# Performance work log

Measured on AMD Instinct MI355X. Metric: run time of the kernel, lower is better.

Reference implementation:

```python
import jax, jax.numpy as jnp
import numpy as np

B, S, H = 1, 4096, 2048
NH, HD = 16, 128
ROPE_N = 32
WINDOW = 1024
EPS = 1e-5


def _build_rope(seq_len, n_elem, base=10000.0):
    theta = 1.0 / (base ** (np.arange(0, n_elem, 2, dtype=np.float32) / n_elem))  # [n_elem/2]
    idx = np.arange(seq_len, dtype=np.float32)
    freqs = np.outer(idx, theta)                     # [S, n_elem/2]
    freqs = np.concatenate([freqs, freqs], axis=-1)  # [S, n_elem]
    return jnp.asarray(np.cos(freqs)), jnp.asarray(np.sin(freqs))


def setup_inputs() -> dict:
    key = jax.random.key(0)
    k1, k2, k3 = jax.random.split(key, 3)
    x = jax.random.normal(k1, (B, S, H), dtype=jnp.float32)
    cos, sin = _build_rope(S, ROPE_N)
    norm_weight = jnp.ones((H,), dtype=jnp.float32)
    qkv_w = jax.random.normal(k2, (3 * H, H), dtype=jnp.float32) * (1.0 / np.sqrt(H))
    o_w = jax.random.normal(k3, (H, H), dtype=jnp.float32) * (1.0 / np.sqrt(H))
    return {"x": x, "cos": cos, "sin": sin, "norm_weight": norm_weight,
            "qkv_w": qkv_w, "o_w": o_w}


def _apply_rope(t, cos, sin):
    # t: [B, NH, S, ROPE_N]; cos/sin: [S, ROPE_N]
    half = t.shape[-1] // 2
    x1, x2 = t[..., :half], t[..., half:]
    rotated = jnp.concatenate([-x2, x1], axis=-1)
    return t * cos + rotated * sin


def reference(x, cos, sin, norm_weight, qkv_w, o_w):
    b, s, h = x.shape
    # RMSNorm (computed in fp32)
    xf = x.astype(jnp.float32)
    ms = jnp.mean(xf * xf, axis=-1, keepdims=True)
    xn = (norm_weight * (xf * jax.lax.rsqrt(ms + EPS))).astype(x.dtype)
    # fused QKV projection
    qkv = jnp.einsum('bsh,oh->bso', xn, qkv_w)  # [B, S, 3H]
    q, k, v = jnp.split(qkv, 3, axis=-1)
    def to_heads(t):
        return t.reshape(b, s, NH, HD).transpose(0, 2, 1, 3)  # [B, NH, S, HD]
    q, k, v = to_heads(q), to_heads(k), to_heads(v)
    # partial RoPE on first ROPE_N dims
    q = jnp.concatenate([_apply_rope(q[..., :ROPE_N], cos, sin), q[..., ROPE_N:]], axis=-1)
    k = jnp.concatenate([_apply_rope(k[..., :ROPE_N], cos, sin), k[..., ROPE_N:]], axis=-1)
    # sliding-window causal attention: query i attends keys j with i-WINDOW <= j <= i
    scale = 1.0 / np.sqrt(HD)
    scores = jnp.einsum('bnqd,bnkd->bnqk', q, k) * scale  # [B, NH, S, S]
    i = jnp.arange(s)[:, None]
    j = jnp.arange(s)[None, :]
    mask = (j <= i) & (j >= i - WINDOW)
    scores = jnp.where(mask, scores, jnp.finfo(scores.dtype).min)
    attn = jax.nn.softmax(scores, axis=-1)
    out = jnp.einsum('bnqk,bnkd->bnqd', attn, v)  # [B, NH, S, HD]
    out = out.transpose(0, 2, 1, 3).reshape(b, s, h)
    return jnp.einsum('bsh,oh->bso', out, o_w)
```

## Files before the change

### kernel.cpp

```cpp
#include <hip/hip_runtime.h>
#include <stdint.h>

#define S_LEN 4096
#define HDIM  2048
#define NHEAD 16
#define HD    128
#define WIN   1024

typedef float  f32x4  __attribute__((ext_vector_type(4)));
typedef float  f32x4v __attribute__((ext_vector_type(4)));
typedef __bf16 bf16x8 __attribute__((ext_vector_type(8)));
typedef short  short8 __attribute__((ext_vector_type(8)));
typedef short  short4v __attribute__((ext_vector_type(4)));

static __device__ __forceinline__ short f2bf(float f) {
  union { float f; uint32_t u; } v; v.f = f;
  uint32_t r = (v.u + 0x7FFFu + ((v.u >> 16) & 1u)) >> 16;
  return (short)(uint16_t)r;
}

static __device__ __forceinline__ void gload_lds16(const void* g, void* l) {
  __builtin_amdgcn_global_load_lds((__attribute__((address_space(1))) void*)g,
                                   (__attribute__((address_space(3))) void*)l,
                                   16, 0, 0);
}

__global__ __launch_bounds__(256) void rmsnorm_k(const float* __restrict__ x,
                                                 const float* __restrict__ w,
                                                 short* __restrict__ xn) {
  const int row = blockIdx.x;
  const int t = threadIdx.x;
  const float* xr = x + (size_t)row * HDIM;
  f32x4v a = *(const f32x4v*)&xr[t * 8];
  f32x4v b = *(const f32x4v*)&xr[t * 8 + 4];
  float ss = a.x*a.x + a.y*a.y + a.z*a.z + a.w*a.w
           + b.x*b.x + b.y*b.y + b.z*b.z + b.w*b.w;
#pragma unroll
  for (int d = 1; d < 64; d <<= 1) ss += __shfl_xor(ss, d, 64);
  __shared__ float sred[4];
  if ((t & 63) == 0) sred[t >> 6] = ss;
  __syncthreads();
  float tot = sred[0] + sred[1] + sred[2] + sred[3];
  float rs = rsqrtf(tot * (1.0f / HDIM) + 1e-5f);
  float vv[8] = {a.x, a.y, a.z, a.w, b.x, b.y, b.z, b.w};
  const float* wp = w + t * 8;
  short8 o;
#pragma unroll
  for (int j = 0; j < 8; ++j) o[j] = f2bf(vv[j] * rs * wp[j]);
  *(short8*)&xn[(size_t)row * HDIM + t * 8] = o;
}

__global__ __launch_bounds__(256) void cvt_k(const float* __restrict__ in,
                                             short* __restrict__ out, int n4) {
  int i = blockIdx.x * 256 + threadIdx.x;
  if (i >= n4) return;
  f32x4v v = *(const f32x4v*)&in[(size_t)i * 4];
  short4v o = { f2bf(v.x), f2bf(v.y), f2bf(v.z), f2bf(v.w) };
  *(short4v*)&out[(size_t)i * 4] = o;
}

template <int EPI>
__global__ __launch_bounds__(256) void gemm_bt(
    const short* __restrict__ A, const short* __restrict__ Bt,
    int M, int N, int K, float* __restrict__ Cf,
    const float* __restrict__ cosb, const float* __restrict__ sinb,
    short* __restrict__ Qo, short* __restrict__ Ko, short* __restrict__ Vt) {
  __shared__ __align__(16) short Al[128 * 64];
  __shared__ __align__(16) short Bl[128 * 64];
  const int t = threadIdx.x;
  const int w = t >> 6, l = t & 63;
  const int lr = l & 15, lg = l >> 4;
  const int wr = w >> 1, wc = w & 1;
  const int brow = blockIdx.y * 128, bcol = blockIdx.x * 128;

  f32x4 acc[4][4] = {};

  const int srow = t >> 3;
  const int scol = (t & 7) * 8;
  const size_t abase = (size_t)(brow + srow) * K + scol;
  const size_t bbase = (size_t)(bcol + srow) * K + scol;

  for (int kt = 0; kt < K; kt += 64) {
#pragma unroll
    for (int i = 0; i < 4; ++i)
      gload_lds16(A + abase + (size_t)(i * 32) * K + kt, &Al[i * 2048 + w * 512]);
#pragma unroll
    for (int i = 0; i < 4; ++i)
      gload_lds16(Bt + bbase + (size_t)(i * 32) * K + kt, &Bl[i * 2048 + w * 512]);
    __syncthreads();
#pragma unroll
    for (int kk = 0; kk < 2; ++kk) {
      bf16x8 af[4], bfm[4];
#pragma unroll
      for (int m = 0; m < 4; ++m)
        af[m] = *(const bf16x8*)&Al[(wr * 64 + m * 16 + lr) * 64 + kk * 32 + lg * 8];
#pragma unroll
      for (int n = 0; n < 4; ++n)
        bfm[n] = *(const bf16x8*)&Bl[(wc * 64 + n * 16 + lr) * 64 + kk * 32 + lg * 8];
#pragma unroll
      for (int m = 0; m < 4; ++m)
#pragma unroll
        for (int n = 0; n < 4; ++n)
          acc[m][n] = __builtin_amdgcn_mfma_f32_16x16x32_bf16(af[m], bfm[n], acc[m][n], 0, 0, 0);
    }
    __syncthreads();
  }

  const int row0 = brow + wr * 64, col0 = bcol + wc * 64;
  if (EPI == 0) {
#pragma unroll
    for (int m = 0; m < 4; ++m)
#pragma unroll
      for (int n = 0; n < 4; ++n)
#pragma unroll
        for (int r = 0; r < 4; ++r)
          Cf[(size_t)(row0 + m * 16 + lg * 4 + r) * N + col0 + n * 16 + lr] = acc[m][n][r];
  } else {
    const int sec = col0 >> 11;
    const int headc = (col0 & 2047) >> 7;
    const bool rope = (sec < 2) && ((col0 & 127) == 0);
#pragma unroll
    for (int m = 0; m < 4; ++m) {
#pragma unroll
      for (int r = 0; r < 4; ++r) {
        const int s = row0 + m * 16 + lg * 4 + r;
        float v0 = acc[m][0][r], v1 = acc[m][1][r];
        float v2 = acc[m][2][r], v3 = acc[m][3][r];
        if (rope) {
          const int d0 = lr;
          float c0 = cosb[s * 32 + d0],      sn0 = sinb[s * 32 + d0];
          float c1 = cosb[s * 32 + d0 + 16], sn1 = sinb[s * 32 + d0 + 16];
          float t0 = v0 * c0 - v1 * sn0;
          float t1 = v1 * c1 + v0 * sn1;
          v0 = t0; v1 = t1;
        }
        float vv[4] = {v0, v1, v2, v3};
#pragma unroll
        for (int n = 0; n < 4; ++n) {
          const int col = col0 + n * 16 + lr;
          const int d = col & 127;
          if (sec == 0)
            Qo[((size_t)headc * S_LEN + s) * HD + d] = f2bf(vv[n] * 0.08838834764831845f);
          else if (sec == 1)
            Ko[((size_t)headc * S_LEN + s) * HD + d] = f2bf(vv[n]);
          else
            Vt[((size_t)headc * HD + d) * S_LEN + s] = f2bf(vv[n]);
        }
      }
    }
  }
}

__global__ __launch_bounds__(256) void attn_k(const short* __restrict__ Q,
                                              const short* __restrict__ Kk,
                                              const short* __restrict__ Vt,
                                              short* __restrict__ Ao) {
  __shared__ __align__(16) short Kl[64 * HD];
  __shared__ __align__(16) short Vl[HD * 64];
  __shared__ __align__(16) short Pl[4][16 * 72];
  const int head = blockIdx.y;
  int bxx = blockIdx.x;
  bxx = ((bxx & 7) << 3) | (bxx >> 3);
  const int qb = bxx * 64;
  const int w = threadIdx.x >> 6, l = threadIdx.x & 63;
  const int lr = l & 15, lg = l >> 4;
  const int q0w = qb + w * 16;
  const short* Qh = Q  + (size_t)head * S_LEN * HD;
  const short* Kh = Kk + (size_t)head * S_LEN * HD;
  const short* Vh = Vt + (size_t)head * HD * S_LEN;

  bf16x8 qf[4];
#pragma unroll
  for (int kk = 0; kk < 4; ++kk)
    qf[kk] = *(const bf16x8*)&Qh[(size_t)(q0w + lr) * HD + kk * 32 + lg * 8];

  f32x4 oacc[8] = {};
  float mrow[4], lrow[4];
#pragma unroll
  for (int r = 0; r < 4; ++r) { mrow[r] = -1e30f; lrow[r] = 0.0f; }

  const int k_begin = (qb >= WIN) ? (qb - WIN) : 0;
  const int nt = (qb + 64 - k_begin) >> 6;
  const int swz = (lr & 7) << 4;

  for (int tkv = 0; tkv < nt; ++tkv) {
    const int k0 = k_begin + tkv * 64;
#pragma unroll
    for (int i = 0; i < 4; ++i) {
      const int row = i * 16 + w * 4 + (l >> 4);
      gload_lds16(Kh + (size_t)(k0 + row) * HD + (((l & 15) ^ (row & 7)) * 8),
                  &Kl[(i * 16 + w * 4) * HD]);
    }
#pragma unroll
    for (int i = 0; i < 4; ++i) {
      const int row = i * 32 + w * 8 + (l >> 3);
      gload_lds16(Vh + (size_t)row * S_LEN + k0 + (((l & 7) ^ (row & 7)) * 8),
                  &Vl[(i * 32 + w * 8) * 64]);
    }
    __syncthreads();

    f32x4 sacc[4] = {};
#pragma unroll
    for (int nf = 0; nf < 4; ++nf) {
      const char* kb = (const char*)Kl + (nf * 16 + lr) * 256;
      bf16x8 kf[4];
#pragma unroll
      for (int kk = 0; kk < 4; ++kk)
        kf[kk] = *(const bf16x8*)(kb + ((kk * 64 + lg * 16) ^ swz));
#pragma unroll
      for (int kk = 0; kk < 4; ++kk)
        sacc[nf] = __builtin_amdgcn_mfma_f32_16x16x32_bf16(qf[kk], kf[nf == nf ? kk : kk], sacc[nf], 0, 0, 0);
    }

    const bool full = (k0 + 63 <= q0w) && (k0 >= q0w + 15 - WIN);
    float scl[4];
#pragma unroll
    for (int r = 0; r < 4; ++r) {
      const int i = q0w + lg * 4 + r;
      float sv[4];
#pragma unroll
      for (int nf = 0; nf < 4; ++nf) sv[nf] = sacc[nf][r];
      if (!full) {
#pragma unroll
        for (int nf = 0; nf < 4; ++nf) {
          const int j = k0 + nf * 16 + lr;
          if (!((j <= i) && (j + WIN >= i))) sv[nf] = -1e30f;
        }
      }
      float mx = fmaxf(fmaxf(sv[0], sv[1]), fmaxf(sv[2], sv[3]));
#pragma unroll
      for (int d = 1; d < 16; d <<= 1) mx = fmaxf(mx, __shfl_xor(mx, d, 64));
      const float mn = fmaxf(mrow[r], mx);
      const float sc = __expf(mrow[r] - mn);
      mrow[r] = mn;
      float p[4], rs = 0.0f;
#pragma unroll
      for (int nf = 0; nf < 4; ++nf) { p[nf] = __expf(sv[nf] - mn); rs += p[nf]; }
#pragma unroll
      for (int d = 1; d < 16; d <<= 1) rs += __shfl_xor(rs, d, 64);
      lrow[r] = lrow[r] * sc + rs;
      scl[r] = sc;
#pragma unroll
      for (int nf = 0; nf < 4; ++nf)
        Pl[w][(lg * 4 + r) * 72 + nf * 16 + lr] = f2bf(p[nf]);
    }
#pragma unroll
    for (int df = 0; df < 8; ++df)
#pragma unroll
      for (int r = 0; r < 4; ++r) oacc[df][r] *= scl[r];

    bf16x8 pa[2];
#pragma unroll
    for (int kk2 = 0; kk2 < 2; ++kk2)
      pa[kk2] = *(const bf16x8*)&Pl[w][lr * 72 + kk2 * 32 + lg * 8];

#pragma unroll
    for (int df = 0; df < 8; ++df) {
      const char* vb = (const char*)Vl + (df * 16 + lr) * 128;
#pragma unroll
      for (int kk2 = 0; kk2 < 2; ++kk2) {
        bf16x8 vfrag = *(const bf16x8*)(vb + ((kk2 * 64 + lg * 16) ^ swz));
        oacc[df] = __builtin_amdgcn_mfma_f32_16x16x32_bf16(pa[kk2], vfrag, oacc[df], 0, 0, 0);
      }
    }
    __syncthreads();
  }

  float inv[4];
#pragma unroll
  for (int r = 0; r < 4; ++r) inv[r] = 1.0f / lrow[r];
#pragma unroll
  for (int df = 0; df < 8; ++df)
#pragma unroll
    for (int r = 0; r < 4; ++r) {
      const int s = q0w + lg * 4 + r;
      Ao[(size_t)s * HDIM + head * HD + df * 16 + lr] = f2bf(oacc[df][r] * inv[r]);
    }
}

extern "C" void kernel_launch(void* const* d_in, const int* in_sizes, int n_in,
                              void* d_out, int out_size, void* d_ws, size_t ws_size,
                              hipStream_t stream) {
  const float* x    = (const float*)d_in[0];
  const float* cosb = (const float*)d_in[1];
  const float* sinb = (const float*)d_in[2];
  const float* nw   = (const float*)d_in[3];
  const float* qkvw = (const float*)d_in[4];
  const float* ow   = (const float*)d_in[5];
  float* out = (float*)d_out;

  short* ws = (short*)d_ws;
  short* xn = ws;
  short* wb = xn + (size_t)S_LEN * HDIM;
  short* Qb = wb + (size_t)3 * HDIM * HDIM;
  short* Kb = Qb + (size_t)NHEAD * S_LEN * HD;
  short* Vb = Kb + (size_t)NHEAD * S_LEN * HD;
  short* Ao = xn;

  rmsnorm_k<<<S_LEN, 256, 0, stream>>>(x, nw, xn);
  cvt_k<<<(3 * HDIM * HDIM / 4 + 255) / 256, 256, 0, stream>>>(qkvw, wb, 3 * HDIM * HDIM / 4);
  gemm_bt<1><<<dim3(3 * HDIM / 128, S_LEN / 128), 256, 0, stream>>>(
      xn, wb, S_LEN, 3 * HDIM, HDIM, nullptr, cosb, sinb, Qb, Kb, Vb);
  cvt_k<<<(HDIM * HDIM / 4 + 255) / 256, 256, 0, stream>>>(ow, wb, HDIM * HDIM / 4);
  attn_k<<<dim3(S_LEN / 64, NHEAD), 256, 0, stream>>>(Qb, Kb, Vb, Ao);
  gemm_bt<0><<<dim3(HDIM / 128, S_LEN / 128), 256, 0, stream>>>(
      Ao, wb, S_LEN, HDIM, HDIM, out, nullptr, nullptr, nullptr, nullptr, nullptr);
}
```

Measured before the change: 351.0 us.

## Replace GEMM with 256x256 tile, 8-wave double-buffered pipelined kernel

Both projection GEMMs now use a 512-thread, 256x256-tile kernel with double-buffered LDS. Global-to-LDS loads for the next tiles are issued during the MFMA phases, gated by explicit vmcnt waits, s_setprio and sched barriers. LDS is XOR-swizzled to avoid bank conflicts, and a 1D grid is remapped so neighbouring blocks share operand tiles in cache. The aim is to hide load latency and raise MFMA utilisation, at the cost of more registers and a fixed 256-tile size assumption. On this shape the output GEMM launches only 128 blocks, which risks underfilling the GPU.

```diff
diff --git a/kernel.cpp b/kernel.cpp
--- a/kernel.cpp
+++ b/kernel.cpp
@@ -60,56 +60,141 @@
 }
 
 template <int EPI>
-__global__ __launch_bounds__(256) void gemm_bt(
+__global__ __launch_bounds__(512, 2) void gemm_8p(
     const short* __restrict__ A, const short* __restrict__ Bt,
     int M, int N, int K, float* __restrict__ Cf,
     const float* __restrict__ cosb, const float* __restrict__ sinb,
     short* __restrict__ Qo, short* __restrict__ Ko, short* __restrict__ Vt) {
-  __shared__ __align__(16) short Al[128 * 64];
-  __shared__ __align__(16) short Bl[128 * 64];
+  __shared__ __align__(16) short lds[2][32768];
   const int t = threadIdx.x;
-  const int w = t >> 6, l = t & 63;
+  const int wid = t >> 6, l = t & 63;
   const int lr = l & 15, lg = l >> 4;
-  const int wr = w >> 1, wc = w & 1;
-  const int brow = blockIdx.y * 128, bcol = blockIdx.x * 128;
-
-  f32x4 acc[4][4] = {};
-
-  const int srow = t >> 3;
-  const int scol = (t & 7) * 8;
-  const size_t abase = (size_t)(brow + srow) * K + scol;
-  const size_t bbase = (size_t)(bcol + srow) * K + scol;
-
-  for (int kt = 0; kt < K; kt += 64) {
-#pragma unroll
-    for (int i = 0; i < 4; ++i)
-      gload_lds16(A + abase + (size_t)(i * 32) * K + kt, &Al[i * 2048 + w * 512]);
-#pragma unroll
-    for (int i = 0; i < 4; ++i)
-      gload_lds16(Bt + bbase + (size_t)(i * 32) * K + kt, &Bl[i * 2048 + w * 512]);
-    __syncthreads();
-#pragma unroll
-    for (int kk = 0; kk < 2; ++kk) {
-      bf16x8 af[4], bfm[4];
-#pragma unroll
-      for (int m = 0; m < 4; ++m)
-        af[m] = *(const bf16x8*)&Al[(wr * 64 + m * 16 + lr) * 64 + kk * 32 + lg * 8];
-#pragma unroll
-      for (int n = 0; n < 4; ++n)
-        bfm[n] = *(const bf16x8*)&Bl[(wc * 64 + n * 16 + lr) * 64 + kk * 32 + lg * 8];
-#pragma unroll
-      for (int m = 0; m < 4; ++m)
-#pragma unroll
-        for (int n = 0; n < 4; ++n)
-          acc[m][n] = __builtin_amdgcn_mfma_f32_16x16x32_bf16(af[m], bfm[n], acc[m][n], 0, 0, 0);
-    }
-    __syncthreads();
+  const int wm = wid >> 2, wn = wid & 3;
+
+  int bid = blockIdx.x;
+  const int nwg = gridDim.x;
+  bid = (bid & 7) * (nwg >> 3) + (bid >> 3);
+  const int nby = M >> 8;
+  const int by = bid % nby, bx = bid / nby;
+  const int brow = by * 256, bcol = bx * 256;
+
+  const int ssl = ((t & 7) ^ ((t >> 3) & 7)) * 8;
+  const short* Asrc = A  + (size_t)(brow + (t >> 3)) * K + ssl;
+  const short* Bsrc = Bt + (size_t)(bcol + (t >> 3)) * K + ssl;
+
+#define ST_A0(d, kt) do {                                                \
+    gload_lds16(Asrc + (size_t)(kt),            &lds[d][t * 8]);         \
+    gload_lds16(Asrc + (size_t)64  * K + (kt),  &lds[d][4096 + t * 8]);  } while (0)
+#define ST_A1(d, kt) do {                                                \
+    gload_lds16(Asrc + (size_t)128 * K + (kt),  &lds[d][8192 + t * 8]);  \
+    gload_lds16(Asrc + (size_t)192 * K + (kt),  &lds[d][12288 + t * 8]); } while (0)
+#define ST_B0(d, kt) do {                                                \
+    gload_lds16(Bsrc + (size_t)(kt),            &lds[d][16384 + t * 8]); \
+    gload_lds16(Bsrc + (size_t)64  * K + (kt),  &lds[d][20480 + t * 8]); } while (0)
+#define ST_B1(d, kt) do {                                                \
+    gload_lds16(Bsrc + (size_t)128 * K + (kt),  &lds[d][24576 + t * 8]); \
+    gload_lds16(Bsrc + (size_t)192 * K + (kt),  &lds[d][28672 + t * 8]); } while (0)
+
+  f32x4 acc[8][4] = {};
+  const int nt = K >> 6;
+
+  const int s0 = ((lg     ) ^ (lr & 7)) * 8;
+  const int s1 = ((lg + 4) ^ (lr & 7)) * 8;
+  const int aB = (wm * 128 + lr) * 64;
+  const int bB = 16384 + (wn * 64 + lr) * 64;
+
+  ST_A0(0, 0); ST_A1(0, 0); ST_B0(0, 0); ST_B1(0, 0);
+  if (nt > 1) { ST_B0(1, 64); ST_A0(1, 64); ST_A1(1, 64); }
+  asm volatile("s_waitcnt vmcnt(6)" ::: "memory");
+  __builtin_amdgcn_s_barrier();
+  __builtin_amdgcn_sched_barrier(0);
+
+  for (int tt = 0; tt < nt; ++tt) {
+    const short* P = &lds[tt & 1][0];
+    bf16x8 a03[4][2], a47[4][2], b01[2][2], b23[2][2];
+
+#pragma unroll
+    for (int m = 0; m < 4; ++m) {
+      a03[m][0] = *(const bf16x8*)&P[aB + m * 1024 + s0];
+      a03[m][1] = *(const bf16x8*)&P[aB + m * 1024 + s1];
+    }
+#pragma unroll
+    for (int n = 0; n < 2; ++n) {
+      b01[n][0] = *(const bf16x8*)&P[bB + n * 1024 + s0];
+      b01[n][1] = *(const bf16x8*)&P[bB + n * 1024 + s1];
+    }
+    if (tt + 1 < nt) ST_B1((tt & 1) ^ 1, (tt + 1) << 6);
+    __builtin_amdgcn_s_setprio(1);
+#pragma unroll
+    for (int m = 0; m < 4; ++m)
+#pragma unroll
+      for (int n = 0; n < 2; ++n) {
+        acc[m][n] = __builtin_amdgcn_mfma_f32_16x16x32_bf16(a03[m][0], b01[n][0], acc[m][n], 0, 0, 0);
+        acc[m][n] = __builtin_amdgcn_mfma_f32_16x16x32_bf16(a03[m][1], b01[n][1], acc[m][n], 0, 0, 0);
+      }
+    __builtin_amdgcn_s_setprio(0);
+
+#pragma unroll
+    for (int n = 0; n < 2; ++n) {
+      b23[n][0] = *(const bf16x8*)&P[bB + (n + 2) * 1024 + s0];
+      b23[n][1] = *(const bf16x8*)&P[bB + (n + 2) * 1024 + s1];
+    }
+    __builtin_amdgcn_s_setprio(1);
+#pragma unroll
+    for (int m = 0; m < 4; ++m)
+#pragma unroll
+      for (int n = 0; n < 2; ++n) {
+        acc[m][n + 2] = __builtin_amdgcn_mfma_f32_16x16x32_bf16(a03[m][0], b23[n][0], acc[m][n + 2], 0, 0, 0);
+        acc[m][n + 2] = __builtin_amdgcn_mfma_f32_16x16x32_bf16(a03[m][1], b23[n][1], acc[m][n + 2], 0, 0, 0);
+      }
+    __builtin_amdgcn_s_setprio(0);
+
+#pragma unroll
+    for (int m = 0; m < 4; ++m) {
+      a47[m][0] = *(const bf16x8*)&P[aB + (m + 4) * 1024 + s0];
+      a47[m][1] = *(const bf16x8*)&P[aB + (m + 4) * 1024 + s1];
+    }
+    __builtin_amdgcn_s_setprio(1);
+#pragma unroll
+    for (int m = 0; m < 4; ++m)
+#pragma unroll
+      for (int n = 0; n < 2; ++n) {
+        acc[m + 4][n + 2] = __builtin_amdgcn_mfma_f32_16x16x32_bf16(a47[m][0], b23[n][0], acc[m + 4][n + 2], 0, 0, 0);
+        acc[m + 4][n + 2] = __builtin_amdgcn_mfma_f32_16x16x32_bf16(a47[m][1], b23[n][1], acc[m + 4][n + 2], 0, 0, 0);
+      }
+    __builtin_amdgcn_s_setprio(0);
+
+    asm volatile("" ::: "memory");
+    __builtin_amdgcn_s_barrier();
+    __builtin_amdgcn_sched_barrier(0);
+
+    if (tt + 2 < nt) {
+      const int k2 = (tt + 2) << 6;
+      ST_B0(tt & 1, k2); ST_A0(tt & 1, k2); ST_A1(tt & 1, k2);
+    }
+    __builtin_amdgcn_s_setprio(1);
+#pragma unroll
+    for (int m = 0; m < 4; ++m)
+#pragma unroll
+      for (int n = 0; n < 2; ++n) {
+        acc[m + 4][n] = __builtin_amdgcn_mfma_f32_16x16x32_bf16(a47[m][0], b01[n][0], acc[m + 4][n], 0, 0, 0);
+        acc[m + 4][n] = __builtin_amdgcn_mfma_f32_16x16x32_bf16(a47[m][1], b01[n][1], acc[m + 4][n], 0, 0, 0);
+      }
+    __builtin_amdgcn_s_setprio(0);
+    if (tt + 2 < nt) asm volatile("s_waitcnt vmcnt(6)" ::: "memory");
+    else             asm volatile("s_waitcnt vmcnt(0)" ::: "memory");
+    __builtin_amdgcn_s_barrier();
+    __builtin_amdgcn_sched_barrier(0);
   }
-
-  const int row0 = brow + wr * 64, col0 = bcol + wc * 64;
+#undef ST_A0
+#undef ST_A1
+#undef ST_B0
+#undef ST_B1
+
+  const int row0 = brow + wm * 128, col0 = bcol + wn * 64;
   if (EPI == 0) {
 #pragma unroll
-    for (int m = 0; m < 4; ++m)
+    for (int m = 0; m < 8; ++m)
 #pragma unroll
       for (int n = 0; n < 4; ++n)
 #pragma unroll
@@ -120,7 +205,7 @@
     const int headc = (col0 & 2047) >> 7;
     const bool rope = (sec < 2) && ((col0 & 127) == 0);
 #pragma unroll
-    for (int m = 0; m < 4; ++m) {
+    for (int m = 0; m < 8; ++m) {
 #pragma unroll
       for (int r = 0; r < 4; ++r) {
         const int s = row0 + m * 16 + lg * 4 + r;
@@ -209,7 +294,7 @@
         kf[kk] = *(const bf16x8*)(kb + ((kk * 64 + lg * 16) ^ swz));
 #pragma unroll
       for (int kk = 0; kk < 4; ++kk)
-        sacc[nf] = __builtin_amdgcn_mfma_f32_16x16x32_bf16(qf[kk], kf[nf == nf ? kk : kk], sacc[nf], 0, 0, 0);
+        sacc[nf] = __builtin_amdgcn_mfma_f32_16x16x32_bf16(qf[kk], kf[kk], sacc[nf], 0, 0, 0);
     }
 
     const bool full = (k0 + 63 <= q0w) && (k0 >= q0w + 15 - WIN);
@@ -299,10 +384,10 @@
 
   rmsnorm_k<<<S_LEN, 256, 0, stream>>>(x, nw, xn);
   cvt_k<<<(3 * HDIM * HDIM / 4 + 255) / 256, 256, 0, stream>>>(qkvw, wb, 3 * HDIM * HDIM / 4);
-  gemm_bt<1><<<dim3(3 * HDIM / 128, S_LEN / 128), 256, 0, stream>>>(
+  gemm_8p<1><<<(S_LEN / 256) * (3 * HDIM / 256), 512, 0, stream>>>(
       xn, wb, S_LEN, 3 * HDIM, HDIM, nullptr, cosb, sinb, Qb, Kb, Vb);
   cvt_k<<<(HDIM * HDIM / 4 + 255) / 256, 256, 0, stream>>>(ow, wb, HDIM * HDIM / 4);
   attn_k<<<dim3(S_LEN / 64, NHEAD), 256, 0, stream>>>(Qb, Kb, Vb, Ao);
-  gemm_bt<0><<<dim3(HDIM / 128, S_LEN / 128), 256, 0, stream>>>(
+  gemm_8p<0><<<(S_LEN / 256) * (HDIM / 256), 512, 0, stream>>>(
       Ao, wb, S_LEN, HDIM, HDIM, out, nullptr, nullptr, nullptr, nullptr, nullptr);
 }
```

After: 337.0 us. 4.0% less time.
